# Kernel tuning notes

Hardware: AMD Instinct MI355X
Metric: run time of the kernel (lower is better)

Reference implementation:

```python
import jax, jax.numpy as jnp
import numpy as np

N_NODES = 50000
N_EDGES = 1600000
N_GRAPHS = 512
VOCAB = 1000
EMB = 32
HID = 64
N_CLASS = 2


def setup_inputs() -> dict:
    key = jax.random.key(0)
    ks = jax.random.split(key, 12)
    x_ids = jax.random.randint(ks[0], (N_NODES,), 0, VOCAB)
    edge_index = jax.random.randint(ks[1], (2, N_EDGES), 0, N_NODES)
    batch = jnp.sort(jax.random.randint(ks[2], (N_NODES,), 0, N_GRAPHS))
    def s(k, shape, fan):
        return jax.random.normal(k, shape, jnp.float32) * (1.0 / np.sqrt(fan))
    return {
        "x_ids": x_ids,
        "edge_index": edge_index,
        "batch": batch,
        "embed": s(ks[3], (VOCAB, EMB), EMB),
        "w1_l": s(ks[4], (EMB, HID), EMB),
        "b1": jnp.zeros((HID,), jnp.float32),
        "w1_r": s(ks[5], (EMB, HID), EMB),
        "w2_l": s(ks[6], (HID, HID), HID),
        "b2": jnp.zeros((HID,), jnp.float32),
        "w2_r": s(ks[7], (HID, HID), HID),
        "w_out": s(ks[8], (HID, N_CLASS), HID),
        "b_out": jnp.zeros((N_CLASS,), jnp.float32),
    }


def _sage(x, src, dst, w_l, b, w_r):
    # PyG SAGEConv (aggr='mean'): out = lin_l(mean_{j in N(i)} x_j) + lin_r(x_i)
    msg_sum = jax.ops.segment_sum(x[src], dst, num_segments=N_NODES)  # [N, d]
    deg = jax.ops.segment_sum(jnp.ones((src.shape[0],), x.dtype), dst,
                              num_segments=N_NODES)
    mean = msg_sum / jnp.maximum(deg, 1.0)[:, None]
    return mean @ w_l + b + x @ w_r


def reference(x_ids, edge_index, batch, embed, w1_l, b1, w1_r,
              w2_l, b2, w2_r, w_out, b_out):
    src, dst = edge_index[0], edge_index[1]
    x = embed[x_ids]                                  # [N, emb]
    x = jax.nn.relu(_sage(x, src, dst, w1_l, b1, w1_r))  # [N, hid]
    x = jax.nn.relu(_sage(x, src, dst, w2_l, b2, w2_r))  # [N, hid]
    # global_mean_pool over batch segments
    gsum = jax.ops.segment_sum(x, batch, num_segments=N_GRAPHS)
    gcnt = jax.ops.segment_sum(jnp.ones((N_NODES,), x.dtype), batch,
                               num_segments=N_GRAPHS)
    pooled = gsum / jnp.maximum(gcnt, 1.0)[:, None]   # [G, hid]
    return pooled @ w_out + b_out                     # [G, n_class]
```

## Files before the change

kernel.cpp:

```cpp
#include <hip/hip_runtime.h>
#include <hip/hip_bf16.h>

#define N_NODES 50000
#define N_EDGES 1600000
#define N_GRAPHS 512
#define VOCAB 1000
#define EMB 32
#define HID 64
#define N_CLASS 2

#define MAXDEG 96

#define NVEC (N_EDGES / 4)
#define SORT_VPB 1024
#define SORT_BLOCKS ((NVEC + SORT_VPB - 1) / SORT_VPB)
#define BSHIFT 7
#define BUCKET_NODES 128
#define NBUCK ((N_NODES + BUCKET_NODES - 1) / BUCKET_NODES)
#define CSR_LSTR 100

#define E1_BLOCKS ((VOCAB * HID + 255) / 256)

#define AGG_THREADS (N_NODES * 8)
#define AGG_BLOCKS ((AGG_THREADS + 255) / 256)

#define L2P_BLOCKS 768
#define L2P_WAVES (L2P_BLOCKS * 4)
#define L2P_CHUNK ((N_NODES + L2P_WAVES - 1) / L2P_WAVES)

typedef int iv4 __attribute__((ext_vector_type(4)));
typedef unsigned short us;
typedef us usv8 __attribute__((ext_vector_type(8)));
typedef float fv4 __attribute__((ext_vector_type(4)));
typedef unsigned long long u64;

__device__ __forceinline__ float bf2f(us u) {
    union { unsigned int i; float f; } c;
    c.i = ((unsigned int)u) << 16;
    return c.f;
}
__device__ __forceinline__ us f2bf(float f) {
    union { __hip_bfloat16 b; us u; } c;
    c.b = __float2bfloat16(f);
    return c.u;
}
__device__ __forceinline__ float rdlane(float v, int k) {
    return __int_as_float(__builtin_amdgcn_readlane(__float_as_int(v), k));
}

__global__ __launch_bounds__(256) void pre_hist_kernel(
        const int* __restrict__ dst, int* __restrict__ hist,
        const float* __restrict__ embed, const float* __restrict__ w1l,
        const float* __restrict__ w1r, us* __restrict__ e1b,
        float* __restrict__ e1r) {
    __shared__ int lh[NBUCK];
    if (blockIdx.x < SORT_BLOCKS) {
        for (int b = threadIdx.x; b < NBUCK; b += 256) lh[b] = 0;
        __syncthreads();
        const iv4* dst4 = (const iv4*)dst;
        int vbase = blockIdx.x * SORT_VPB;
        #pragma unroll
        for (int t = 0; t < 4; ++t) {
            int v = vbase + t * 256 + threadIdx.x;
            if (v < NVEC) {
                iv4 d4 = __builtin_nontemporal_load(&dst4[v]);
                atomicAdd(&lh[d4.x >> BSHIFT], 1);
                atomicAdd(&lh[d4.y >> BSHIFT], 1);
                atomicAdd(&lh[d4.z >> BSHIFT], 1);
                atomicAdd(&lh[d4.w >> BSHIFT], 1);
            }
        }
        __syncthreads();
        for (int b = threadIdx.x; b < NBUCK; b += 256)
            hist[b * SORT_BLOCKS + blockIdx.x] = lh[b];
    } else {
        int id = (blockIdx.x - SORT_BLOCKS) * 256 + threadIdx.x;
        if (id >= VOCAB * HID) return;
        int v = id >> 6, j = id & 63;
        float a = 0.0f, b = 0.0f;
        #pragma unroll
        for (int k = 0; k < EMB; ++k) {
            float ev = embed[v * EMB + k];
            a = fmaf(ev, w1l[k * HID + j], a);
            b = fmaf(ev, w1r[k * HID + j], b);
        }
        e1b[id] = f2bf(a);
        e1r[id] = b;
    }
}

__global__ __launch_bounds__(256) void scan_rows_kernel(int* __restrict__ hist,
                                                        int* __restrict__ btot) {
    int* row = hist + (size_t)blockIdx.x * SORT_BLOCKS;
    __shared__ int wsum[4];
    int tid = threadIdx.x, lane = tid & 63, w = tid >> 6;
    int carry = 0;
    for (int base = 0; base < SORT_BLOCKS; base += 256) {
        int idx = base + tid;
        int v = (idx < SORT_BLOCKS) ? row[idx] : 0;
        int inc = v;
        #pragma unroll
        for (int off = 1; off < 64; off <<= 1) {
            int n = __shfl_up(inc, off, 64);
            if (lane >= off) inc += n;
        }
        if (lane == 63) wsum[w] = inc;
        __syncthreads();
        int woff = 0;
        #pragma unroll
        for (int k = 0; k < 4; ++k) if (k < w) woff += wsum[k];
        if (idx < SORT_BLOCKS) row[idx] = carry + woff + inc - v;
        carry += wsum[0] + wsum[1] + wsum[2] + wsum[3];
        __syncthreads();
    }
    if (tid == 0) btot[blockIdx.x] = carry;
}

__global__ __launch_bounds__(256) void scatter_kernel(const int* __restrict__ src,
        const int* __restrict__ dst, const int* __restrict__ x_ids,
        const int* __restrict__ hist, const int* __restrict__ btot,
        int* __restrict__ boff, u64* __restrict__ ebuf) {
    __shared__ int lbase[NBUCK];
    __shared__ int wsum[4];
    int tid = threadIdx.x, lane = tid & 63, w = tid >> 6;
    int carry = 0;
    for (int base = 0; base < NBUCK; base += 256) {
        int idx = base + tid;
        int v = (idx < NBUCK) ? btot[idx] : 0;
        int inc = v;
        #pragma unroll
        for (int off = 1; off < 64; off <<= 1) {
            int n = __shfl_up(inc, off, 64);
            if (lane >= off) inc += n;
        }
        if (lane == 63) wsum[w] = inc;
        __syncthreads();
        int woff = 0;
        #pragma unroll
        for (int k = 0; k < 4; ++k) if (k < w) woff += wsum[k];
        if (idx < NBUCK) lbase[idx] = carry + woff + inc - v;
        carry += wsum[0] + wsum[1] + wsum[2] + wsum[3];
        __syncthreads();
    }
    for (int b = tid; b < NBUCK; b += 256) {
        if (blockIdx.x == 0) boff[b] = lbase[b];
        lbase[b] += hist[b * SORT_BLOCKS + blockIdx.x];
    }
    if (blockIdx.x == 0 && tid == 0) boff[NBUCK] = carry;
    __syncthreads();
    const iv4* dst4 = (const iv4*)dst;
    const iv4* src4 = (const iv4*)src;
    int vbase = blockIdx.x * SORT_VPB;
    #pragma unroll
    for (int t = 0; t < 4; ++t) {
        int v = vbase + t * 256 + threadIdx.x;
        if (v < NVEC) {
            iv4 d4 = __builtin_nontemporal_load(&dst4[v]);
            iv4 s4 = __builtin_nontemporal_load(&src4[v]);
            int pay0 = (x_ids[s4.x] << 16) | s4.x;
            int pay1 = (x_ids[s4.y] << 16) | s4.y;
            int pay2 = (x_ids[s4.z] << 16) | s4.z;
            int pay3 = (x_ids[s4.w] << 16) | s4.w;
            int p0 = atomicAdd(&lbase[d4.x >> BSHIFT], 1);
            int p1 = atomicAdd(&lbase[d4.y >> BSHIFT], 1);
            int p2 = atomicAdd(&lbase[d4.z >> BSHIFT], 1);
            int p3 = atomicAdd(&lbase[d4.w >> BSHIFT], 1);
            ebuf[p0] = ((u64)(unsigned)d4.x << 32) | (unsigned)pay0;
            ebuf[p1] = ((u64)(unsigned)d4.y << 32) | (unsigned)pay1;
            ebuf[p2] = ((u64)(unsigned)d4.z << 32) | (unsigned)pay2;
            ebuf[p3] = ((u64)(unsigned)d4.w << 32) | (unsigned)pay3;
        }
    }
}

__global__ __launch_bounds__(256) void csr_agg1_kernel(const u64* __restrict__ ebuf,
        const int* __restrict__ boff, int* __restrict__ cursor, int* __restrict__ csr,
        const int* __restrict__ x_ids, const us* __restrict__ e1b,
        const float* __restrict__ e1r, const float* __restrict__ b1,
        float* __restrict__ h1, us* __restrict__ h1b, float* __restrict__ gsum) {
    __shared__ int csr_l[BUCKET_NODES * CSR_LSTR];
    __shared__ int cur[BUCKET_NODES];
    int b = blockIdx.x;
    int tid = threadIdx.x;
    for (int r = tid; r < BUCKET_NODES; r += 256) cur[r] = 0;
    if (b < 128) gsum[b * 256 + tid] = 0.0f;
    __syncthreads();
    int base = boff[b];
    int end  = boff[b + 1];
    int node0 = b << BSHIFT;
    for (int i = base + tid; i < end; i += 256) {
        u64 e = ebuf[i];
        int d = (int)(e >> 32);
        int pay = (int)(e & 0xffffffffu);
        int r = d - node0;
        int pos = atomicAdd(&cur[r], 1);
        csr_l[r * CSR_LSTR + pos] = pay;
        csr[(size_t)d * MAXDEG + pos] = pay;
    }
    __syncthreads();
    for (int r = tid; r < BUCKET_NODES; r += 256) {
        int d = node0 + r;
        if (d < N_NODES) cursor[d] = cur[r];
    }
    int lane = tid & 63;
    int wv = tid >> 6;
    int g = lane >> 3, c8 = lane & 7;
    for (int slot = wv * 8 + g; slot < BUCKET_NODES; slot += 32) {
        int node = node0 + slot;
        bool valid = node < N_NODES;
        int deg = valid ? cur[slot] : 0;
        const int* crow = csr_l + slot * CSR_LSTR;
        float a0=0.f,a1=0.f,a2=0.f,a3=0.f,a4=0.f,a5=0.f,a6=0.f,a7=0.f;
        for (int k = 0; k < deg; k += 4) {
            iv4 cv = *(const iv4*)(crow + k);
            #define GATH1(CVAL, T)                                                   \
            if (k + (T) < deg) {                                                     \
                int cls = (CVAL) >> 16;                                              \
                usv8 r = *(const usv8*)(e1b + cls * HID + c8 * 8);                   \
                a0 += bf2f(r[0]); a1 += bf2f(r[1]); a2 += bf2f(r[2]); a3 += bf2f(r[3]); \
                a4 += bf2f(r[4]); a5 += bf2f(r[5]); a6 += bf2f(r[6]); a7 += bf2f(r[7]); \
            }
            GATH1(cv.x, 0) GATH1(cv.y, 1) GATH1(cv.z, 2) GATH1(cv.w, 3)
            #undef GATH1
        }
        if (!valid) continue;
        float inv = 1.0f / fmaxf((float)deg, 1.0f);
        int xid = x_ids[node];
        const fv4* er = (const fv4*)(e1r + xid * HID + c8 * 8);
        fv4 e0 = er[0], e1v = er[1];
        const fv4* bb = (const fv4*)(b1 + c8 * 8);
        fv4 b0 = bb[0], b1v = bb[1];
        fv4 h0, h1v;
        h0.x = fmaxf(a0 * inv + b0.x + e0.x, 0.0f);
        h0.y = fmaxf(a1 * inv + b0.y + e0.y, 0.0f);
        h0.z = fmaxf(a2 * inv + b0.z + e0.z, 0.0f);
        h0.w = fmaxf(a3 * inv + b0.w + e0.w, 0.0f);
        h1v.x = fmaxf(a4 * inv + b1v.x + e1v.x, 0.0f);
        h1v.y = fmaxf(a5 * inv + b1v.y + e1v.y, 0.0f);
        h1v.z = fmaxf(a6 * inv + b1v.z + e1v.z, 0.0f);
        h1v.w = fmaxf(a7 * inv + b1v.w + e1v.w, 0.0f);
        int o = node * HID + c8 * 8;
        *(fv4*)(h1 + o) = h0;
        *(fv4*)(h1 + o + 4) = h1v;
        usv8 hb;
        hb[0] = f2bf(h0.x); hb[1] = f2bf(h0.y); hb[2] = f2bf(h0.z); hb[3] = f2bf(h0.w);
        hb[4] = f2bf(h1v.x); hb[5] = f2bf(h1v.y); hb[6] = f2bf(h1v.z); hb[7] = f2bf(h1v.w);
        *(usv8*)(h1b + o) = hb;
    }
}

__global__ __launch_bounds__(256) void agg2_mean_kernel(
        const us* __restrict__ h1b, const int* __restrict__ csr,
        const int* __restrict__ deg_arr, float* __restrict__ mean2) {
    int tid = blockIdx.x * blockDim.x + threadIdx.x;
    int lane = threadIdx.x & 63;
    int g = lane >> 3, c8 = lane & 7;
    int node = (tid >> 6) * 8 + g;
    bool valid = node < N_NODES;
    int nclamp = valid ? node : 0;
    int deg = valid ? deg_arr[nclamp] : 0;
    const int* crow = csr + (size_t)nclamp * MAXDEG;
    float a0=0.f,a1=0.f,a2=0.f,a3=0.f,a4=0.f,a5=0.f,a6=0.f,a7=0.f;
    for (int k = 0; k < deg; k += 4) {
        iv4 cv = *(const iv4*)(crow + k);
        #define GATH2(CVAL, T)                                                   \
        if (k + (T) < deg) {                                                     \
            int nb = (CVAL) & 0xFFFF;                                            \
            usv8 r = *(const usv8*)(h1b + nb * HID + c8 * 8);                    \
            a0 += bf2f(r[0]); a1 += bf2f(r[1]); a2 += bf2f(r[2]); a3 += bf2f(r[3]); \
            a4 += bf2f(r[4]); a5 += bf2f(r[5]); a6 += bf2f(r[6]); a7 += bf2f(r[7]); \
        }
        GATH2(cv.x, 0) GATH2(cv.y, 1) GATH2(cv.z, 2) GATH2(cv.w, 3)
        #undef GATH2
    }
    if (!valid) return;
    float inv = 1.0f / fmaxf((float)deg, 1.0f);
    fv4 m0, m1;
    m0.x = a0 * inv; m0.y = a1 * inv; m0.z = a2 * inv; m0.w = a3 * inv;
    m1.x = a4 * inv; m1.y = a5 * inv; m1.z = a6 * inv; m1.w = a7 * inv;
    int o = node * HID + c8 * 8;
    *(fv4*)(mean2 + o) = m0;
    *(fv4*)(mean2 + o + 4) = m1;
}

__global__ __launch_bounds__(256) void lin2_pool_kernel(
        const float* __restrict__ mean2, const float* __restrict__ h1,
        const float* __restrict__ w2l, const float* __restrict__ b2,
        const float* __restrict__ w2r, const int* __restrict__ batch,
        float* __restrict__ gsum) {
    int lane = threadIdx.x & 63;
    int wv = (blockIdx.x * blockDim.x + threadIdx.x) >> 6;
    int i0 = wv * L2P_CHUNK;
    int i1 = i0 + L2P_CHUNK; if (i1 > N_NODES) i1 = N_NODES;
    if (i0 >= N_NODES) return;
    float wl[HID], wr[HID];
    #pragma unroll
    for (int k = 0; k < HID; ++k) {
        wl[k] = w2l[k * HID + lane];
        wr[k] = w2r[k * HID + lane];
    }
    float bj = b2[lane];
    int curg = __builtin_amdgcn_readfirstlane(batch[i0]);
    float accp = 0.0f;
    float m = mean2[i0 * HID + lane];
    float h = h1[i0 * HID + lane];
    for (int i = i0; i < i1; ++i) {
        float mn = 0.f, hn = 0.f;
        if (i + 1 < i1) {
            mn = mean2[(i + 1) * HID + lane];
            hn = h1[(i + 1) * HID + lane];
        }
        int g = __builtin_amdgcn_readfirstlane(batch[i]);
        if (g != curg) {
            atomicAdd(&gsum[curg * HID + lane], accp);
            accp = 0.0f;
            curg = g;
        }
        float z = bj;
        #pragma unroll
        for (int k = 0; k < HID; ++k)
            z = fmaf(rdlane(m, k), wl[k], fmaf(rdlane(h, k), wr[k], z));
        accp += fmaxf(z, 0.0f);
        m = mn; h = hn;
    }
    atomicAdd(&gsum[curg * HID + lane], accp);
}

__global__ void out_kernel(const float* __restrict__ gsum, const int* __restrict__ batch,
                           const float* __restrict__ w_out, const float* __restrict__ b_out,
                           float* __restrict__ out) {
    int id = blockIdx.x * blockDim.x + threadIdx.x;
    if (id >= N_GRAPHS * N_CLASS) return;
    int g = id >> 1, c = id & 1;
    int lo = 0, hi = N_NODES;
    while (lo < hi) { int mid = (lo + hi) >> 1; if (batch[mid] < g) lo = mid + 1; else hi = mid; }
    int first = lo;
    lo = 0; hi = N_NODES;
    while (lo < hi) { int mid = (lo + hi) >> 1; if (batch[mid] <= g) lo = mid + 1; else hi = mid; }
    float cnt = (float)(lo - first);
    float inv = 1.0f / fmaxf(cnt, 1.0f);
    float acc = b_out[c];
    #pragma unroll
    for (int j = 0; j < HID; ++j)
        acc = fmaf(gsum[g * HID + j] * inv, w_out[j * N_CLASS + c], acc);
    out[id] = acc;
}


extern "C" void kernel_launch(void* const* d_in, const int* in_sizes, int n_in,
                              void* d_out, int out_size, void* d_ws, size_t ws_size,
                              hipStream_t stream) {
    const int*   x_ids = (const int*)d_in[0];
    const int*   edge  = (const int*)d_in[1];
    const int*   batch = (const int*)d_in[2];
    const float* embed = (const float*)d_in[3];
    const float* w1l   = (const float*)d_in[4];
    const float* b1    = (const float*)d_in[5];
    const float* w1r   = (const float*)d_in[6];
    const float* w2l   = (const float*)d_in[7];
    const float* b2    = (const float*)d_in[8];
    const float* w2r   = (const float*)d_in[9];
    const float* wout  = (const float*)d_in[10];
    const float* bout  = (const float*)d_in[11];
    const int* src = edge;
    const int* dst = edge + N_EDGES;
    float* out = (float*)d_out;

    char* ws = (char*)d_ws;
    size_t off = 0;
    auto alloc = [&](size_t bytes) -> void* {
        void* p = ws + off;
        off += (bytes + 255) & ~(size_t)255;
        return p;
    };
    float*  h1     = (float*)alloc((size_t)N_NODES * HID * 4);
    us*     h1b    = (us*)alloc((size_t)N_NODES * HID * 2);
    u64*    ebuf   = (u64*)alloc((size_t)N_EDGES * 8);
    int*    csr    = (int*)alloc((size_t)N_NODES * MAXDEG * 4);
    int*    cursor = (int*)alloc((size_t)N_NODES * 4);
    int*    hist   = (int*)alloc((size_t)NBUCK * SORT_BLOCKS * 4);
    int*    btot   = (int*)alloc((size_t)NBUCK * 4);
    int*    boff   = (int*)alloc((size_t)(NBUCK + 1) * 4);
    us*     e1b    = (us*)alloc((size_t)VOCAB * HID * 2);
    float*  e1r    = (float*)alloc((size_t)VOCAB * HID * 4);
    float*  gsum   = (float*)alloc((size_t)N_GRAPHS * HID * 4);

    float* mean2 = (float*)ebuf;

    const int B = 256;
    pre_hist_kernel<<<SORT_BLOCKS + E1_BLOCKS, B, 0, stream>>>(dst, hist,
                                                               embed, w1l, w1r, e1b, e1r);
    scan_rows_kernel<<<NBUCK, B, 0, stream>>>(hist, btot);
    scatter_kernel<<<SORT_BLOCKS, B, 0, stream>>>(src, dst, x_ids, hist, btot, boff, ebuf);
    csr_agg1_kernel<<<NBUCK, B, 0, stream>>>(ebuf, boff, cursor, csr,
                                             x_ids, e1b, e1r, b1, h1, h1b, gsum);
    agg2_mean_kernel<<<AGG_BLOCKS, B, 0, stream>>>(h1b, csr, cursor, mean2);
    lin2_pool_kernel<<<L2P_BLOCKS, B, 0, stream>>>(mean2, h1, w2l, b2, w2r, batch, gsum);
    out_kernel<<<(N_GRAPHS * N_CLASS + B - 1) / B, B, 0, stream>>>(gsum, batch, wout, bout, out);
}
```

Before: 241.8 us.

## Split CSR bucket build from layer-1 aggregation into separate kernels

The fused bucket kernel that built the CSR in shared memory (about 51KB LDS per block) and then aggregated layer-1 embeddings is split in two. One kernel only places edges into the global CSR and writes degrees, and a new grid-wide kernel gathers from the global CSR the same way agg2 does. This removes the large LDS footprint that limited occupancy to about 391 blocks and lets layer-1 aggregation spread over many more waves. In exchange it adds a kernel launch and re-reads the CSR from global memory or L2 instead of LDS.

```diff
diff --git a/kernel.cpp b/kernel.cpp
--- a/kernel.cpp
+++ b/kernel.cpp
@@ -17,7 +17,6 @@
 #define BSHIFT 7
 #define BUCKET_NODES 128
 #define NBUCK ((N_NODES + BUCKET_NODES - 1) / BUCKET_NODES)
-#define CSR_LSTR 100
 
 #define E1_BLOCKS ((VOCAB * HID + 255) / 256)
 
@@ -173,15 +172,12 @@
     }
 }
 
-__global__ __launch_bounds__(256) void csr_agg1_kernel(const u64* __restrict__ ebuf,
+__global__ __launch_bounds__(256) void csr_bucket_kernel(const u64* __restrict__ ebuf,
         const int* __restrict__ boff, int* __restrict__ cursor, int* __restrict__ csr,
-        const int* __restrict__ x_ids, const us* __restrict__ e1b,
-        const float* __restrict__ e1r, const float* __restrict__ b1,
-        float* __restrict__ h1, us* __restrict__ h1b, float* __restrict__ gsum) {
-    __shared__ int csr_l[BUCKET_NODES * CSR_LSTR];
-    __shared__ int cur[BUCKET_NODES];
+        float* __restrict__ gsum) {
     int b = blockIdx.x;
     int tid = threadIdx.x;
+    __shared__ int cur[BUCKET_NODES];
     for (int r = tid; r < BUCKET_NODES; r += 256) cur[r] = 0;
     if (b < 128) gsum[b * 256 + tid] = 0.0f;
     __syncthreads();
@@ -192,9 +188,7 @@
         u64 e = ebuf[i];
         int d = (int)(e >> 32);
         int pay = (int)(e & 0xffffffffu);
-        int r = d - node0;
-        int pos = atomicAdd(&cur[r], 1);
-        csr_l[r * CSR_LSTR + pos] = pay;
+        int pos = atomicAdd(&cur[d - node0], 1);
         csr[(size_t)d * MAXDEG + pos] = pay;
     }
     __syncthreads();
@@ -202,51 +196,57 @@
         int d = node0 + r;
         if (d < N_NODES) cursor[d] = cur[r];
     }
-    int lane = tid & 63;
-    int wv = tid >> 6;
+}
+
+__global__ __launch_bounds__(256) void agg1_lin1_kernel(
+        const int* __restrict__ x_ids, const int* __restrict__ csr,
+        const int* __restrict__ deg_arr, const us* __restrict__ e1b,
+        const float* __restrict__ e1r, const float* __restrict__ b1,
+        float* __restrict__ h1, us* __restrict__ h1b) {
+    int tid = blockIdx.x * blockDim.x + threadIdx.x;
+    int lane = threadIdx.x & 63;
     int g = lane >> 3, c8 = lane & 7;
-    for (int slot = wv * 8 + g; slot < BUCKET_NODES; slot += 32) {
-        int node = node0 + slot;
-        bool valid = node < N_NODES;
-        int deg = valid ? cur[slot] : 0;
-        const int* crow = csr_l + slot * CSR_LSTR;
-        float a0=0.f,a1=0.f,a2=0.f,a3=0.f,a4=0.f,a5=0.f,a6=0.f,a7=0.f;
-        for (int k = 0; k < deg; k += 4) {
-            iv4 cv = *(const iv4*)(crow + k);
-            #define GATH1(CVAL, T)                                                   \
-            if (k + (T) < deg) {                                                     \
-                int cls = (CVAL) >> 16;                                              \
-                usv8 r = *(const usv8*)(e1b + cls * HID + c8 * 8);                   \
-                a0 += bf2f(r[0]); a1 += bf2f(r[1]); a2 += bf2f(r[2]); a3 += bf2f(r[3]); \
-                a4 += bf2f(r[4]); a5 += bf2f(r[5]); a6 += bf2f(r[6]); a7 += bf2f(r[7]); \
-            }
-            GATH1(cv.x, 0) GATH1(cv.y, 1) GATH1(cv.z, 2) GATH1(cv.w, 3)
-            #undef GATH1
-        }
-        if (!valid) continue;
-        float inv = 1.0f / fmaxf((float)deg, 1.0f);
-        int xid = x_ids[node];
-        const fv4* er = (const fv4*)(e1r + xid * HID + c8 * 8);
-        fv4 e0 = er[0], e1v = er[1];
-        const fv4* bb = (const fv4*)(b1 + c8 * 8);
-        fv4 b0 = bb[0], b1v = bb[1];
-        fv4 h0, h1v;
-        h0.x = fmaxf(a0 * inv + b0.x + e0.x, 0.0f);
-        h0.y = fmaxf(a1 * inv + b0.y + e0.y, 0.0f);
-        h0.z = fmaxf(a2 * inv + b0.z + e0.z, 0.0f);
-        h0.w = fmaxf(a3 * inv + b0.w + e0.w, 0.0f);
-        h1v.x = fmaxf(a4 * inv + b1v.x + e1v.x, 0.0f);
-        h1v.y = fmaxf(a5 * inv + b1v.y + e1v.y, 0.0f);
-        h1v.z = fmaxf(a6 * inv + b1v.z + e1v.z, 0.0f);
-        h1v.w = fmaxf(a7 * inv + b1v.w + e1v.w, 0.0f);
-        int o = node * HID + c8 * 8;
-        *(fv4*)(h1 + o) = h0;
-        *(fv4*)(h1 + o + 4) = h1v;
-        usv8 hb;
-        hb[0] = f2bf(h0.x); hb[1] = f2bf(h0.y); hb[2] = f2bf(h0.z); hb[3] = f2bf(h0.w);
-        hb[4] = f2bf(h1v.x); hb[5] = f2bf(h1v.y); hb[6] = f2bf(h1v.z); hb[7] = f2bf(h1v.w);
-        *(usv8*)(h1b + o) = hb;
-    }
+    int node = (tid >> 6) * 8 + g;
+    bool valid = node < N_NODES;
+    int nclamp = valid ? node : 0;
+    int deg = valid ? deg_arr[nclamp] : 0;
+    const int* crow = csr + (size_t)nclamp * MAXDEG;
+    float a0=0.f,a1=0.f,a2=0.f,a3=0.f,a4=0.f,a5=0.f,a6=0.f,a7=0.f;
+    for (int k = 0; k < deg; k += 4) {
+        iv4 cv = *(const iv4*)(crow + k);
+        #define GATH1(CVAL, T)                                                   \
+        if (k + (T) < deg) {                                                     \
+            int cls = (CVAL) >> 16;                                              \
+            usv8 r = *(const usv8*)(e1b + cls * HID + c8 * 8);                   \
+            a0 += bf2f(r[0]); a1 += bf2f(r[1]); a2 += bf2f(r[2]); a3 += bf2f(r[3]); \
+            a4 += bf2f(r[4]); a5 += bf2f(r[5]); a6 += bf2f(r[6]); a7 += bf2f(r[7]); \
+        }
+        GATH1(cv.x, 0) GATH1(cv.y, 1) GATH1(cv.z, 2) GATH1(cv.w, 3)
+        #undef GATH1
+    }
+    if (!valid) return;
+    float inv = 1.0f / fmaxf((float)deg, 1.0f);
+    int xid = x_ids[nclamp];
+    const fv4* er = (const fv4*)(e1r + xid * HID + c8 * 8);
+    fv4 e0 = er[0], e1v = er[1];
+    const fv4* bb = (const fv4*)(b1 + c8 * 8);
+    fv4 b0 = bb[0], b1v = bb[1];
+    fv4 h0, h1v;
+    h0.x = fmaxf(a0 * inv + b0.x + e0.x, 0.0f);
+    h0.y = fmaxf(a1 * inv + b0.y + e0.y, 0.0f);
+    h0.z = fmaxf(a2 * inv + b0.z + e0.z, 0.0f);
+    h0.w = fmaxf(a3 * inv + b0.w + e0.w, 0.0f);
+    h1v.x = fmaxf(a4 * inv + b1v.x + e1v.x, 0.0f);
+    h1v.y = fmaxf(a5 * inv + b1v.y + e1v.y, 0.0f);
+    h1v.z = fmaxf(a6 * inv + b1v.z + e1v.z, 0.0f);
+    h1v.w = fmaxf(a7 * inv + b1v.w + e1v.w, 0.0f);
+    int o = node * HID + c8 * 8;
+    *(fv4*)(h1 + o) = h0;
+    *(fv4*)(h1 + o + 4) = h1v;
+    usv8 hb;
+    hb[0] = f2bf(h0.x); hb[1] = f2bf(h0.y); hb[2] = f2bf(h0.z); hb[3] = f2bf(h0.w);
+    hb[4] = f2bf(h1v.x); hb[5] = f2bf(h1v.y); hb[6] = f2bf(h1v.z); hb[7] = f2bf(h1v.w);
+    *(usv8*)(h1b + o) = hb;
 }
 
 __global__ __launch_bounds__(256) void agg2_mean_kernel(
@@ -392,8 +392,9 @@
                                                                embed, w1l, w1r, e1b, e1r);
     scan_rows_kernel<<<NBUCK, B, 0, stream>>>(hist, btot);
     scatter_kernel<<<SORT_BLOCKS, B, 0, stream>>>(src, dst, x_ids, hist, btot, boff, ebuf);
-    csr_agg1_kernel<<<NBUCK, B, 0, stream>>>(ebuf, boff, cursor, csr,
-                                             x_ids, e1b, e1r, b1, h1, h1b, gsum);
+    csr_bucket_kernel<<<NBUCK, B, 0, stream>>>(ebuf, boff, cursor, csr, gsum);
+    agg1_lin1_kernel<<<AGG_BLOCKS, B, 0, stream>>>(x_ids, csr, cursor,
+                                                   e1b, e1r, b1, h1, h1b);
     agg2_mean_kernel<<<AGG_BLOCKS, B, 0, stream>>>(h1b, csr, cursor, mean2);
     lin2_pool_kernel<<<L2P_BLOCKS, B, 0, stream>>>(mean2, h1, w2l, b2, w2r, batch, gsum);
     out_kernel<<<(N_GRAPHS * N_CLASS + B - 1) / B, B, 0, stream>>>(gsum, batch, wout, bout, out);
```

Measured after the change: 225.8 us. -6.6%, faster.
